# Kernel tuning notes

Measured on AMD Instinct MI355X. Metric: run time of the kernel, lower is better.

Reference implementation:

```python
import jax, jax.numpy as jnp
import numpy as np

H, D, TS, A, R, TR = 256, 2, 32, 4, 16, 8  # h_size, max_output_degree, t_size, n_aggr, rank, t_rank
BS = 16384


def setup_inputs() -> dict:
    key = jax.random.key(0)
    ks = jax.random.split(key, 9)
    return {
        "neighbour_h": jax.random.normal(ks[0], (BS, D, H), jnp.float32),
        "type_embs": jax.random.normal(ks[1], (BS, TS), jnp.float32),
        # per-child input projections U: (max_output_degree, n_aggr, h_size, rank)
        "U": jax.random.normal(ks[2], (D, A, H, R), jnp.float32) * 0.05,
        "b": jax.random.normal(ks[3], (D, A, 1, R), jnp.float32) * 0.05,
        # type projection
        "U_type": jax.random.normal(ks[4], (TS, A * TR), jnp.float32) * 0.05,
        "b_type": jax.random.normal(ks[5], (1, A * TR), jnp.float32) * 0.05,
        # stacked augmented core tensors T_list: (n_aggr, t_rank+1, rank+1, rank+1, rank)
        "T": jax.random.normal(ks[6], (A, TR + 1, R + 1, R + 1, R), jnp.float32) * 0.02,
        # output projection
        "U_output": jax.random.normal(ks[7], (A, R, H), jnp.float32) * 0.05,
        "b_output": jax.random.normal(ks[8], (A, 1, H), jnp.float32) * 0.05,
    }


def _aug(x):
    # append a constant-1 feature along the last dim: (bs, a, d) -> (bs, a, d+1)
    bs, a, _ = x.shape
    return jnp.concatenate([x, jnp.ones((bs, a, 1), x.dtype)], axis=-1)


def reference(neighbour_h, type_embs, U, b, U_type, b_type, T, U_output, b_output):
    # child projections: (bs, n_ch, n_aggr, rank)
    ch = jnp.einsum('bch,cahr->bcar', neighbour_h, U) + b[:, :, 0, :]
    # type projection: (bs, n_aggr, t_rank)
    tp = (type_embs @ U_type + b_type).reshape(-1, A, TR)
    # augmented (homogeneous) inputs
    h0 = _aug(tp)         # (bs, a, TR+1)
    h1 = _aug(ch[:, 0])   # (bs, a, R+1)
    h2 = _aug(ch[:, 1])   # (bs, a, R+1)
    # sequential multilinear (Tucker/HOSVD) contraction with the core tensor,
    # vectorized over batch and aggregators (original loops over n_aggr)
    r = jnp.einsum('bap,apqrs->baqrs', h0, T)
    r = jnp.einsum('baq,baqrs->bars', h1, r)
    g = jnp.einsum('bar,bars->bas', h2, r)            # (bs, a, R)
    out = jnp.einsum('bar,arh->bah', g, U_output) + b_output[:, 0, :]
    return out.reshape(neighbour_h.shape[0], -1)      # (bs, n_aggr*h_size)
```

## Files before the change

### kernel.cpp

```cpp
#include <hip/hip_runtime.h>

#define NTHR 512
#define TB 32

typedef __attribute__((ext_vector_type(8))) short bf16x8;
typedef __attribute__((ext_vector_type(4))) float f32x4;
typedef float4 f4;
typedef unsigned short u16;

__device__ __forceinline__ u16 f2b(float x) {
  union { float f; unsigned u; } v; v.f = x;
  unsigned r = (v.u + 0x7fffu + ((v.u >> 16) & 1u)) >> 16;
  return (u16)r;
}
__device__ __forceinline__ float b2f(u16 u) {
  union { unsigned u; float f; } v; v.u = ((unsigned)u) << 16;
  return v.f;
}
__device__ __forceinline__ unsigned pack2(float a, float b) {
  return (unsigned)f2b(a) | ((unsigned)f2b(b) << 16);
}
__device__ __forceinline__ unsigned cvtpk(float lo, float hi) {
  unsigned r;
  asm("v_cvt_pk_bf16_f32 %0, %1, %2" : "=v"(r) : "v"(lo), "v"(hi));
  return r;
}
__device__ __forceinline__ float blo(unsigned u) {
  union { unsigned u; float f; } v; v.u = u << 16; return v.f;
}
__device__ __forceinline__ float bhi(unsigned u) {
  union { unsigned u; float f; } v; v.u = u & 0xffff0000u; return v.f;
}

extern "C" __global__ void hosvd_prep(const float* __restrict__ U,
                                      const float* __restrict__ T,
                                      const float* __restrict__ UO,
                                      unsigned* __restrict__ ws32) {
  int id = blockIdx.x * 256 + threadIdx.x;
  if (id < 92160) {
    int j2 = id & 3, frag = id >> 2;
    int l = frag & 63, f2 = frag >> 6;
    int p = f2 % 9, akt = f2 / 9;
    int kt = akt % 10, a = akt / 10;
    int s = l & 15;
    float v[2];
    #pragma unroll
    for (int j = 0; j < 2; ++j) {
      int kp = kt * 32 + (l >> 4) * 8 + j2 * 2 + j;
      float x = 0.f;
      if (kp < 306) {
        int q = (unsigned)kp / 18u, r = kp - q * 18;
        if (r < 17) x = T[(((a * 9 + p) * 17 + q) * 17 + r) * 16 + s];
      }
      v[j] = x;
    }
    ws32[id] = pack2(v[0], v[1]);
  } else if (id < 108544) {
    int rel = id - 92160;
    int j2 = rel & 3, frag = rel >> 2;
    int l = frag & 63, f2 = frag >> 6;
    int kt = f2 & 7, g = f2 >> 3;
    int a = g & 3, c = g >> 2;
    int rr = l & 15;
    int k = kt * 32 + (l >> 4) * 8 + j2 * 2;
    float v0 = U[((c * 4 + a) * 256 + k + 0) * 16 + rr];
    float v1 = U[((c * 4 + a) * 256 + k + 1) * 16 + rr];
    ws32[id] = pack2(v0, v1);
  } else if (id < 124928) {
    int rel = id - 108544;
    int j2 = rel & 3, frag = rel >> 2;
    int l = frag & 63, f2 = frag >> 6;
    int ht = f2 & 15, a = f2 >> 4;
    int h = ht * 16 + (l & 15);
    int k = (l >> 4) * 8 + j2 * 2;
    float v0 = (k + 0 < 16) ? UO[(a * 16 + k + 0) * 256 + h] : 0.f;
    float v1 = (k + 1 < 16) ? UO[(a * 16 + k + 1) * 256 + h] : 0.f;
    ws32[id] = pack2(v0, v1);
  }
}

#define MFMA_B(A, B, C) __builtin_amdgcn_mfma_f32_16x16x32_bf16(A, B, C, 0, 0, 0)

#define LOADP(DST, P, KTN)                                                   \
  do {                                                                       \
    _Pragma("unroll")                                                        \
    for (int kk = 0; kk < (KTN); ++kk)                                       \
      DST[kk] = *(const bf16x8*)&BTf[(size_t)((a * 10 + kt0 + kk) * 9 + (P)) * 512 + l * 8]; \
  } while (0)

#define DOP(BSET, P, KTN)                                                    \
  do {                                                                       \
    f32x4 c0_ = {0.f, 0.f, 0.f, 0.f}, c1_ = {0.f, 0.f, 0.f, 0.f};            \
    _Pragma("unroll")                                                        \
    for (int kk = 0; kk < (KTN); ++kk) {                                     \
      c0_ = MFMA_B(Af0[kk], BSET[kk], c0_);                                  \
      c1_ = MFMA_B(Af1[kk], BSET[kk], c1_);                                  \
    }                                                                        \
    f4 tv0_ = *(const f4*)&s_tpt[(a * 9 + (P)) * 32 + 4 * q];                \
    f4 tv1_ = *(const f4*)&s_tpt[(a * 9 + (P)) * 32 + 16 + 4 * q];           \
    gp0[0] = fmaf(tv0_.x, c0_[0], gp0[0]);                                   \
    gp0[1] = fmaf(tv0_.y, c0_[1], gp0[1]);                                   \
    gp0[2] = fmaf(tv0_.z, c0_[2], gp0[2]);                                   \
    gp0[3] = fmaf(tv0_.w, c0_[3], gp0[3]);                                   \
    gp1[0] = fmaf(tv1_.x, c1_[0], gp1[0]);                                   \
    gp1[1] = fmaf(tv1_.y, c1_[1], gp1[1]);                                   \
    gp1[2] = fmaf(tv1_.z, c1_[2], gp1[2]);                                   \
    gp1[3] = fmaf(tv1_.w, c1_[3], gp1[3]);                                   \
  } while (0)

#define CORE_GEMM(KTN)                                                       \
  do {                                                                       \
    const u16* oa_ = &s_u[aL * 10496];                                       \
    bf16x8 Af0[KTN], Af1[KTN];                                               \
    _Pragma("unroll")                                                        \
    for (int kk = 0; kk < (KTN); ++kk) {                                     \
      Af0[kk] = *(const bf16x8*)&oa_[rl * 328 + (kt0 + kk) * 32 + 8 * q];    \
      Af1[kk] = *(const bf16x8*)&oa_[(16 + rl) * 328 + (kt0 + kk) * 32 + 8 * q]; \
    }                                                                        \
    bf16x8 Ba[KTN], Bb[KTN], Bc[KTN];                                        \
    LOADP(Ba, 0, KTN); LOADP(Bb, 1, KTN); LOADP(Bc, 2, KTN);                 \
    DOP(Ba, 0, KTN); LOADP(Ba, 3, KTN);                                      \
    DOP(Bb, 1, KTN); LOADP(Bb, 4, KTN);                                      \
    DOP(Bc, 2, KTN); LOADP(Bc, 5, KTN);                                      \
    DOP(Ba, 3, KTN); LOADP(Ba, 6, KTN);                                      \
    DOP(Bb, 4, KTN); LOADP(Bb, 7, KTN);                                      \
    DOP(Bc, 5, KTN); LOADP(Bc, 8, KTN);                                      \
    DOP(Ba, 6, KTN);                                                         \
    DOP(Bb, 7, KTN);                                                         \
    DOP(Bc, 8, KTN);                                                         \
  } while (0)

extern "C" __global__ __launch_bounds__(NTHR, 4)
void hosvd_main(const float* __restrict__ nh, const float* __restrict__ te,
                const float* __restrict__ bw, const float* __restrict__ Ut,
                const float* __restrict__ bt, const float* __restrict__ bO,
                const u16* __restrict__ BTf, const u16* __restrict__ UcTf,
                const u16* __restrict__ UOTf, float* __restrict__ out) {
  __shared__ __align__(16) u16   s_u[20992];
  __shared__ __align__(16) u16   s_ch[TB * 164];
  __shared__ __align__(16) float s_tpt[36 * 32];
  __shared__ __align__(16) u16   s_g[TB * 136];
  __shared__ __align__(16) float s_red[3264];

  const int t = threadIdx.x;
  const int ib0 = blockIdx.x * TB;
  const int w = t >> 6, l = t & 63;
  const int rl = l & 15, q = l >> 4;

  {
    const int row = t >> 4, cc = (t >> 3) & 1, aa = (t >> 1) & 3, sl = t & 1;
    s_ch[row * 164 + cc * 80 + aa * 20 + 16 + sl] = sl ? (u16)0 : (u16)0x3F80;
  }
  if (t < 128) {
    const int aa = t >> 5, row = t & 31;
    s_tpt[(aa * 9 + 8) * 32 + row] = 1.0f;
  }

  if (t < 256) {
    const int row = t >> 3, k4 = t & 7;
    f4 v = *(const f4*)&te[(size_t)(ib0 + row) * 32 + k4 * 4];
    float* d = &s_red[row * 33 + k4 * 4];
    d[0] = v.x; d[1] = v.y; d[2] = v.z; d[3] = v.w;
  } else {
    const int j = t - 256;
    *(f4*)&s_red[1056 + j * 4] = *(const f4*)&Ut[j * 4];
  }
  for (int lp = t; lp < 4096; lp += NTHR) {
    const int row = lp >> 7, rem = lp & 127;
    const int c = rem >> 6, k0 = (rem & 63) * 4;
    f4 v = *(const f4*)&nh[((size_t)(ib0 + row) * 2 + c) * 256 + k0];
    *(uint2*)&s_u[row * 520 + c * 256 + k0] =
        make_uint2(cvtpk(v.x, v.y), cvtpk(v.z, v.w));
  }
  __syncthreads();

  {
    const int i = t >> 4, o = t & 15;
    const int off = o * 2;
    const int aa = off >> 3, p0 = off & 7;
    float acc0 = bt[off], acc1 = bt[off + 1];
    #pragma unroll
    for (int k = 0; k < 32; ++k) {
      float tv = s_red[i * 33 + k];
      float2 u = *(const float2*)&s_red[1056 + k * 32 + off];
      acc0 = fmaf(tv, u.x, acc0);
      acc1 = fmaf(tv, u.y, acc1);
    }
    s_tpt[(aa * 9 + p0) * 32 + i]     = acc0;
    s_tpt[(aa * 9 + p0 + 1) * 32 + i] = acc1;
  }

  {
    const int c = w >> 2, a = w & 3;
    const u16* u0 = &UcTf[((size_t)((c * 4 + a) * 8) * 64 + l) * 8];
    bf16x8 C0 = *(const bf16x8*)(u0 + 0 * 512);
    bf16x8 C1 = *(const bf16x8*)(u0 + 1 * 512);
    bf16x8 C2 = *(const bf16x8*)(u0 + 2 * 512);
    bf16x8 C3 = *(const bf16x8*)(u0 + 3 * 512);
    bf16x8 C4 = *(const bf16x8*)(u0 + 4 * 512);
    bf16x8 C5 = *(const bf16x8*)(u0 + 5 * 512);
    bf16x8 C6 = *(const bf16x8*)(u0 + 6 * 512);
    bf16x8 C7 = *(const bf16x8*)(u0 + 7 * 512);
    f32x4 ac0 = {0.f, 0.f, 0.f, 0.f}, ac1 = {0.f, 0.f, 0.f, 0.f};
    #define PCKT(KT, CB)                                                          \
    {                                                                             \
      bf16x8 A0_ = *(const bf16x8*)&s_u[rl * 520 + c * 256 + KT * 32 + 8 * q];    \
      bf16x8 A1_ = *(const bf16x8*)&s_u[(16 + rl) * 520 + c * 256 + KT * 32 + 8 * q]; \
      ac0 = MFMA_B(A0_, CB, ac0);                                                 \
      ac1 = MFMA_B(A1_, CB, ac1);                                                 \
    }
    PCKT(0, C0) PCKT(1, C1) PCKT(2, C2) PCKT(3, C3)
    PCKT(4, C4) PCKT(5, C5) PCKT(6, C6) PCKT(7, C7)
    #undef PCKT
    const float bias = bw[(c * 4 + a) * 16 + rl];
    #pragma unroll
    for (int reg = 0; reg < 4; ++reg) {
      s_ch[(4 * q + reg) * 164 + c * 80 + a * 20 + rl]      = f2b(ac0[reg] + bias);
      s_ch[(16 + 4 * q + reg) * 164 + c * 80 + a * 20 + rl] = f2b(ac1[reg] + bias);
    }
  }
  __syncthreads();

  const int aL = w >> 2;
  const int kq = w & 3;
  const int kt0 = (kq <= 2) ? kq * 3 : 8;

  for (int it = 0; it < 2; ++it) {
    const int aB = it * 2;
    const int a = aB + aL;

    for (int lp = t; lp < 1152; lp += NTHR) {
      const int row = lp & 31, rest = lp >> 5;
      const int aLb = (rest >= 18) ? 1 : 0;
      const int qv = rest - aLb * 18;
      const int ab = aB + aLb;
      const float h1f = b2f(s_ch[row * 164 + ab * 20 + qv]);
      const u16* h2p = &s_ch[row * 164 + 80 + ab * 20];
      uint2 ha = *(const uint2*)&h2p[0];
      uint2 hb = *(const uint2*)&h2p[4];
      uint2 hc = *(const uint2*)&h2p[8];
      uint2 hd = *(const uint2*)&h2p[12];
      unsigned he = *(const unsigned*)&h2p[16];
      unsigned* op = (unsigned*)&s_u[aLb * 10496 + row * 328 + qv * 18];
      op[0] = cvtpk(h1f * blo(ha.x), h1f * bhi(ha.x));
      op[1] = cvtpk(h1f * blo(ha.y), h1f * bhi(ha.y));
      op[2] = cvtpk(h1f * blo(hb.x), h1f * bhi(hb.x));
      op[3] = cvtpk(h1f * blo(hb.y), h1f * bhi(hb.y));
      op[4] = cvtpk(h1f * blo(hc.x), h1f * bhi(hc.x));
      op[5] = cvtpk(h1f * blo(hc.y), h1f * bhi(hc.y));
      op[6] = cvtpk(h1f * blo(hd.x), h1f * bhi(hd.x));
      op[7] = cvtpk(h1f * blo(hd.y), h1f * bhi(hd.y));
      op[8] = cvtpk(h1f * blo(he),   h1f * bhi(he));
    }
    __syncthreads();

    f32x4 gp0 = {0.f, 0.f, 0.f, 0.f}, gp1 = {0.f, 0.f, 0.f, 0.f};
    __builtin_amdgcn_s_setprio(1);
    if (kq < 2) { CORE_GEMM(3); } else { CORE_GEMM(2); }
    __builtin_amdgcn_s_setprio(0);

    if (kq) {
      #pragma unroll
      for (int reg = 0; reg < 4; ++reg) {
        s_red[((kq - 1) * 2 + aL) * 544 + (4 * q + reg) * 17 + rl]       = gp0[reg];
        s_red[((kq - 1) * 2 + aL) * 544 + 272 + (4 * q + reg) * 17 + rl] = gp1[reg];
      }
    }
    __syncthreads();

    if (kq == 0) {
      #pragma unroll
      for (int mm = 0; mm < 2; ++mm)
        #pragma unroll
        for (int reg = 0; reg < 4; ++reg) {
          const int idx = aL * 544 + mm * 272 + (4 * q + reg) * 17 + rl;
          float g = (mm ? gp1[reg] : gp0[reg]) +
                    s_red[idx] + s_red[1088 + idx] + s_red[2176 + idx];
          const int row = mm * 16 + 4 * q + reg;
          s_g[row * 136 + a * 32 + rl]      = f2b(g);
          s_g[row * 136 + a * 32 + 16 + rl] = 0;
        }
    }
  }
  __syncthreads();

  {
    const int e = w;
    #pragma unroll
    for (int a = 0; a < 4; ++a) {
      const u16* ub = &UOTf[((size_t)(a * 16 + e * 2) * 64 + l) * 8];
      bf16x8 E0 = *(const bf16x8*)(ub);
      bf16x8 E1 = *(const bf16x8*)(ub + 512);
      bf16x8 A0 = *(const bf16x8*)&s_g[rl * 136 + a * 32 + 8 * q];
      bf16x8 A1 = *(const bf16x8*)&s_g[(16 + rl) * 136 + a * 32 + 8 * q];
      const float b0 = bO[a * 256 + (e * 2 + 0) * 16 + rl];
      const float b1 = bO[a * 256 + (e * 2 + 1) * 16 + rl];
      f32x4 e00 = {b0, b0, b0, b0}, e01 = e00;
      f32x4 e10 = {b1, b1, b1, b1}, e11 = e10;
      e00 = MFMA_B(A0, E0, e00);
      e01 = MFMA_B(A1, E0, e01);
      e10 = MFMA_B(A0, E1, e10);
      e11 = MFMA_B(A1, E1, e11);
      #pragma unroll
      for (int reg = 0; reg < 4; ++reg) {
        const size_t r0 = (size_t)(ib0 + 4 * q + reg) * 1024 + a * 256;
        const size_t r1 = (size_t)(ib0 + 16 + 4 * q + reg) * 1024 + a * 256;
        out[r0 + (e * 2 + 0) * 16 + rl] = e00[reg];
        out[r1 + (e * 2 + 0) * 16 + rl] = e01[reg];
        out[r0 + (e * 2 + 1) * 16 + rl] = e10[reg];
        out[r1 + (e * 2 + 1) * 16 + rl] = e11[reg];
      }
    }
  }
}

extern "C" void kernel_launch(void* const* d_in, const int* in_sizes, int n_in,
                              void* d_out, int out_size, void* d_ws, size_t ws_size,
                              hipStream_t stream) {
  const float* nh = (const float*)d_in[0];
  const float* te = (const float*)d_in[1];
  const float* U  = (const float*)d_in[2];
  const float* bw = (const float*)d_in[3];
  const float* Ut = (const float*)d_in[4];
  const float* bt = (const float*)d_in[5];
  const float* T  = (const float*)d_in[6];
  const float* UO = (const float*)d_in[7];
  const float* bO = (const float*)d_in[8];
  float* out = (float*)d_out;

  unsigned* ws32 = (unsigned*)d_ws;
  hipLaunchKernelGGL(hosvd_prep, dim3(488), dim3(256), 0, stream, U, T, UO, ws32);

  const u16* BTf  = (const u16*)d_ws;
  const u16* UcTf = BTf + 184320;
  const u16* UOTf = UcTf + 32768;

  const int bs = in_sizes[0] / 512;
  hipLaunchKernelGGL(hosvd_main, dim3(bs / TB), dim3(NTHR), 0, stream,
                     nh, te, bw, Ut, bt, bO, BTf, UcTf, UOTf, out);
}
```

Baseline: 44.33 us.

## Build core-GEMM A fragments in registers and split work by aggregator and row-half

```diff
diff --git a/kernel.cpp b/kernel.cpp
--- a/kernel.cpp
+++ b/kernel.cpp
@@ -24,12 +24,6 @@
   unsigned r;
   asm("v_cvt_pk_bf16_f32 %0, %1, %2" : "=v"(r) : "v"(lo), "v"(hi));
   return r;
-}
-__device__ __forceinline__ float blo(unsigned u) {
-  union { unsigned u; float f; } v; v.u = u << 16; return v.f;
-}
-__device__ __forceinline__ float bhi(unsigned u) {
-  union { unsigned u; float f; } v; v.u = u & 0xffff0000u; return v.f;
 }
 
 extern "C" __global__ void hosvd_prep(const float* __restrict__ U,
@@ -81,75 +75,28 @@
 
 #define MFMA_B(A, B, C) __builtin_amdgcn_mfma_f32_16x16x32_bf16(A, B, C, 0, 0, 0)
 
-#define LOADP(DST, P, KTN)                                                   \
-  do {                                                                       \
-    _Pragma("unroll")                                                        \
-    for (int kk = 0; kk < (KTN); ++kk)                                       \
-      DST[kk] = *(const bf16x8*)&BTf[(size_t)((a * 10 + kt0 + kk) * 9 + (P)) * 512 + l * 8]; \
-  } while (0)
-
-#define DOP(BSET, P, KTN)                                                    \
-  do {                                                                       \
-    f32x4 c0_ = {0.f, 0.f, 0.f, 0.f}, c1_ = {0.f, 0.f, 0.f, 0.f};            \
-    _Pragma("unroll")                                                        \
-    for (int kk = 0; kk < (KTN); ++kk) {                                     \
-      c0_ = MFMA_B(Af0[kk], BSET[kk], c0_);                                  \
-      c1_ = MFMA_B(Af1[kk], BSET[kk], c1_);                                  \
-    }                                                                        \
-    f4 tv0_ = *(const f4*)&s_tpt[(a * 9 + (P)) * 32 + 4 * q];                \
-    f4 tv1_ = *(const f4*)&s_tpt[(a * 9 + (P)) * 32 + 16 + 4 * q];           \
-    gp0[0] = fmaf(tv0_.x, c0_[0], gp0[0]);                                   \
-    gp0[1] = fmaf(tv0_.y, c0_[1], gp0[1]);                                   \
-    gp0[2] = fmaf(tv0_.z, c0_[2], gp0[2]);                                   \
-    gp0[3] = fmaf(tv0_.w, c0_[3], gp0[3]);                                   \
-    gp1[0] = fmaf(tv1_.x, c1_[0], gp1[0]);                                   \
-    gp1[1] = fmaf(tv1_.y, c1_[1], gp1[1]);                                   \
-    gp1[2] = fmaf(tv1_.z, c1_[2], gp1[2]);                                   \
-    gp1[3] = fmaf(tv1_.w, c1_[3], gp1[3]);                                   \
-  } while (0)
-
-#define CORE_GEMM(KTN)                                                       \
-  do {                                                                       \
-    const u16* oa_ = &s_u[aL * 10496];                                       \
-    bf16x8 Af0[KTN], Af1[KTN];                                               \
-    _Pragma("unroll")                                                        \
-    for (int kk = 0; kk < (KTN); ++kk) {                                     \
-      Af0[kk] = *(const bf16x8*)&oa_[rl * 328 + (kt0 + kk) * 32 + 8 * q];    \
-      Af1[kk] = *(const bf16x8*)&oa_[(16 + rl) * 328 + (kt0 + kk) * 32 + 8 * q]; \
-    }                                                                        \
-    bf16x8 Ba[KTN], Bb[KTN], Bc[KTN];                                        \
-    LOADP(Ba, 0, KTN); LOADP(Bb, 1, KTN); LOADP(Bc, 2, KTN);                 \
-    DOP(Ba, 0, KTN); LOADP(Ba, 3, KTN);                                      \
-    DOP(Bb, 1, KTN); LOADP(Bb, 4, KTN);                                      \
-    DOP(Bc, 2, KTN); LOADP(Bc, 5, KTN);                                      \
-    DOP(Ba, 3, KTN); LOADP(Ba, 6, KTN);                                      \
-    DOP(Bb, 4, KTN); LOADP(Bb, 7, KTN);                                      \
-    DOP(Bc, 5, KTN); LOADP(Bc, 8, KTN);                                      \
-    DOP(Ba, 6, KTN);                                                         \
-    DOP(Bb, 7, KTN);                                                         \
-    DOP(Bc, 8, KTN);                                                         \
-  } while (0)
-
 extern "C" __global__ __launch_bounds__(NTHR, 4)
 void hosvd_main(const float* __restrict__ nh, const float* __restrict__ te,
                 const float* __restrict__ bw, const float* __restrict__ Ut,
                 const float* __restrict__ bt, const float* __restrict__ bO,
                 const u16* __restrict__ BTf, const u16* __restrict__ UcTf,
                 const u16* __restrict__ UOTf, float* __restrict__ out) {
-  __shared__ __align__(16) u16   s_u[20992];
+  __shared__ __align__(16) u16   s_u[18688];
   __shared__ __align__(16) u16   s_ch[TB * 164];
   __shared__ __align__(16) float s_tpt[36 * 32];
   __shared__ __align__(16) u16   s_g[TB * 136];
-  __shared__ __align__(16) float s_red[3264];
 
   const int t = threadIdx.x;
   const int ib0 = blockIdx.x * TB;
   const int w = t >> 6, l = t & 63;
   const int rl = l & 15, q = l >> 4;
 
-  {
-    const int row = t >> 4, cc = (t >> 3) & 1, aa = (t >> 1) & 3, sl = t & 1;
-    s_ch[row * 164 + cc * 80 + aa * 20 + 16 + sl] = sl ? (u16)0 : (u16)0x3F80;
+  float* teL = (float*)s_g;
+  float* UtL = (float*)&s_u[16640];
+
+  if (t < 256) {
+    const int row = t >> 3, cc = (t >> 2) & 1, aa = t & 3;
+    *(uint2*)&s_ch[row * 164 + cc * 80 + aa * 20 + 16] = make_uint2(0x3F80u, 0u);
   }
   if (t < 128) {
     const int aa = t >> 5, row = t & 31;
@@ -159,11 +106,11 @@
   if (t < 256) {
     const int row = t >> 3, k4 = t & 7;
     f4 v = *(const f4*)&te[(size_t)(ib0 + row) * 32 + k4 * 4];
-    float* d = &s_red[row * 33 + k4 * 4];
+    float* d = &teL[row * 33 + k4 * 4];
     d[0] = v.x; d[1] = v.y; d[2] = v.z; d[3] = v.w;
   } else {
     const int j = t - 256;
-    *(f4*)&s_red[1056 + j * 4] = *(const f4*)&Ut[j * 4];
+    *(f4*)&UtL[j * 4] = *(const f4*)&Ut[j * 4];
   }
   for (int lp = t; lp < 4096; lp += NTHR) {
     const int row = lp >> 7, rem = lp & 127;
@@ -181,8 +128,8 @@
     float acc0 = bt[off], acc1 = bt[off + 1];
     #pragma unroll
     for (int k = 0; k < 32; ++k) {
-      float tv = s_red[i * 33 + k];
-      float2 u = *(const float2*)&s_red[1056 + k * 32 + off];
+      float tv = teL[i * 33 + k];
+      float2 u = *(const float2*)&UtL[k * 32 + off];
       acc0 = fmaf(tv, u.x, acc0);
       acc1 = fmaf(tv, u.y, acc1);
     }
@@ -221,65 +168,77 @@
   }
   __syncthreads();
 
-  const int aL = w >> 2;
-  const int kq = w & 3;
-  const int kt0 = (kq <= 2) ? kq * 3 : 8;
-
-  for (int it = 0; it < 2; ++it) {
-    const int aB = it * 2;
-    const int a = aB + aL;
-
-    for (int lp = t; lp < 1152; lp += NTHR) {
-      const int row = lp & 31, rest = lp >> 5;
-      const int aLb = (rest >= 18) ? 1 : 0;
-      const int qv = rest - aLb * 18;
-      const int ab = aB + aLb;
-      const float h1f = b2f(s_ch[row * 164 + ab * 20 + qv]);
-      const u16* h2p = &s_ch[row * 164 + 80 + ab * 20];
-      uint2 ha = *(const uint2*)&h2p[0];
-      uint2 hb = *(const uint2*)&h2p[4];
-      uint2 hc = *(const uint2*)&h2p[8];
-      uint2 hd = *(const uint2*)&h2p[12];
-      unsigned he = *(const unsigned*)&h2p[16];
-      unsigned* op = (unsigned*)&s_u[aLb * 10496 + row * 328 + qv * 18];
-      op[0] = cvtpk(h1f * blo(ha.x), h1f * bhi(ha.x));
-      op[1] = cvtpk(h1f * blo(ha.y), h1f * bhi(ha.y));
-      op[2] = cvtpk(h1f * blo(hb.x), h1f * bhi(hb.x));
-      op[3] = cvtpk(h1f * blo(hb.y), h1f * bhi(hb.y));
-      op[4] = cvtpk(h1f * blo(hc.x), h1f * bhi(hc.x));
-      op[5] = cvtpk(h1f * blo(hc.y), h1f * bhi(hc.y));
-      op[6] = cvtpk(h1f * blo(hd.x), h1f * bhi(hd.x));
-      op[7] = cvtpk(h1f * blo(hd.y), h1f * bhi(hd.y));
-      op[8] = cvtpk(h1f * blo(he),   h1f * bhi(he));
-    }
-    __syncthreads();
-
-    f32x4 gp0 = {0.f, 0.f, 0.f, 0.f}, gp1 = {0.f, 0.f, 0.f, 0.f};
+  {
+    const int a = w & 3, m = w >> 2;
+    const int row = m * 16 + rl;
+    const u16* h1g = &s_ch[row * 164 + a * 20];
+    const u16* h2g = &s_ch[row * 164 + 80 + a * 20];
+
+    f32x4 acc[9];
+    #pragma unroll
+    for (int p = 0; p < 9; ++p) acc[p] = (f32x4){0.f, 0.f, 0.f, 0.f};
+
     __builtin_amdgcn_s_setprio(1);
-    if (kq < 2) { CORE_GEMM(3); } else { CORE_GEMM(2); }
+    #pragma unroll
+    for (int kt = 0; kt < 10; ++kt) {
+      const u16* bp = &BTf[(size_t)((a * 10 + kt) * 9) * 512 + l * 8];
+      bf16x8 B0 = *(const bf16x8*)(bp + 0 * 512);
+      bf16x8 B1 = *(const bf16x8*)(bp + 1 * 512);
+      bf16x8 B2 = *(const bf16x8*)(bp + 2 * 512);
+      bf16x8 B3 = *(const bf16x8*)(bp + 3 * 512);
+      bf16x8 B4 = *(const bf16x8*)(bp + 4 * 512);
+      bf16x8 B5 = *(const bf16x8*)(bp + 5 * 512);
+      bf16x8 B6 = *(const bf16x8*)(bp + 6 * 512);
+      bf16x8 B7 = *(const bf16x8*)(bp + 7 * 512);
+      bf16x8 B8 = *(const bf16x8*)(bp + 8 * 512);
+
+      const int k0 = kt * 32 + 8 * q;
+      const unsigned qq0 = (unsigned)k0 / 18u;
+      const int rr0 = k0 - (int)qq0 * 18;
+      const int brk = 18 - rr0;
+      const float h1a = b2f(h1g[qq0]);
+      const float h1b = b2f(h1g[qq0 + 1]);
+      float hv[8];
+      #pragma unroll
+      for (int j = 0; j < 8; ++j) {
+        int rr = rr0 + j;
+        rr = (rr >= 18) ? rr - 18 : rr;
+        const float h2v = b2f(h2g[rr]);
+        const float h1v = (j < brk) ? h1a : h1b;
+        hv[j] = h1v * h2v;
+      }
+      union { unsigned u[4]; bf16x8 v; } Au;
+      Au.u[0] = cvtpk(hv[0], hv[1]);
+      Au.u[1] = cvtpk(hv[2], hv[3]);
+      Au.u[2] = cvtpk(hv[4], hv[5]);
+      Au.u[3] = cvtpk(hv[6], hv[7]);
+
+      acc[0] = MFMA_B(Au.v, B0, acc[0]);
+      acc[1] = MFMA_B(Au.v, B1, acc[1]);
+      acc[2] = MFMA_B(Au.v, B2, acc[2]);
+      acc[3] = MFMA_B(Au.v, B3, acc[3]);
+      acc[4] = MFMA_B(Au.v, B4, acc[4]);
+      acc[5] = MFMA_B(Au.v, B5, acc[5]);
+      acc[6] = MFMA_B(Au.v, B6, acc[6]);
+      acc[7] = MFMA_B(Au.v, B7, acc[7]);
+      acc[8] = MFMA_B(Au.v, B8, acc[8]);
+    }
     __builtin_amdgcn_s_setprio(0);
 
-    if (kq) {
-      #pragma unroll
-      for (int reg = 0; reg < 4; ++reg) {
-        s_red[((kq - 1) * 2 + aL) * 544 + (4 * q + reg) * 17 + rl]       = gp0[reg];
-        s_red[((kq - 1) * 2 + aL) * 544 + 272 + (4 * q + reg) * 17 + rl] = gp1[reg];
-      }
-    }
-    __syncthreads();
-
-    if (kq == 0) {
-      #pragma unroll
-      for (int mm = 0; mm < 2; ++mm)
-        #pragma unroll
-        for (int reg = 0; reg < 4; ++reg) {
-          const int idx = aL * 544 + mm * 272 + (4 * q + reg) * 17 + rl;
-          float g = (mm ? gp1[reg] : gp0[reg]) +
-                    s_red[idx] + s_red[1088 + idx] + s_red[2176 + idx];
-          const int row = mm * 16 + 4 * q + reg;
-          s_g[row * 136 + a * 32 + rl]      = f2b(g);
-          s_g[row * 136 + a * 32 + 16 + rl] = 0;
-        }
+    float gp[4] = {0.f, 0.f, 0.f, 0.f};
+    #pragma unroll
+    for (int p = 0; p < 9; ++p) {
+      f4 tv = *(const f4*)&s_tpt[(a * 9 + p) * 32 + m * 16 + 4 * q];
+      gp[0] = fmaf(tv.x, acc[p][0], gp[0]);
+      gp[1] = fmaf(tv.y, acc[p][1], gp[1]);
+      gp[2] = fmaf(tv.z, acc[p][2], gp[2]);
+      gp[3] = fmaf(tv.w, acc[p][3], gp[3]);
+    }
+    #pragma unroll
+    for (int reg = 0; reg < 4; ++reg) {
+      const int row2 = m * 16 + 4 * q + reg;
+      s_g[row2 * 136 + a * 32 + rl]      = f2b(gp[reg]);
+      s_g[row2 * 136 + a * 32 + 16 + rl] = 0;
     }
   }
   __syncthreads();
```

Measured after the change: 41.49 us. 1.07x faster.
